# Kernel optimization log

Measured on AMD Instinct MI355X. Metric: run time of the kernel, lower is better.

Reference implementation:

```python
import jax, jax.numpy as jnp
import numpy as np

B, N, N2 = 4, 4096, 4096
CIN, DIM, KNN, UP = 128, 64, 20, 2
HPOS, HATT = 64, 256
EPS = 1e-5


def _group(feat, idx):
    # feat: (B,C,M), idx: (B,N,K) -> (B,C,N,K) gather of neighbor features
    return jax.vmap(lambda f, i: f[:, i])(feat, idx)


def _conv1d(w, b, x):
    # 1x1 Conv1d: w (O,C), x (B,C,N)
    return jnp.einsum('oc,bcn->bon', w, x) + b[:, None]


def _bn(x, g, be, m, v):
    # eval-mode BatchNorm2d on (B,C,N,K)
    inv = g / jnp.sqrt(v + EPS)
    return x * inv[:, None, None] + (be - m * inv)[:, None, None]


def setup_inputs() -> dict:
    key = jax.random.key(0)
    ks = jax.random.split(key, 32)
    r = lambda i, s: jax.random.normal(ks[i], s, jnp.float32)
    u = lambda i, s: jax.random.uniform(ks[i], s, jnp.float32, 0.5, 1.5)
    return {
        'pos1': r(0, (B, 3, N)),
        'query': r(1, (B, CIN, N)),
        'pos2': r(2, (B, 3, N2)),
        'key_feat': r(3, (B, CIN, N2)),
        'wq': r(4, (DIM, CIN)) * 0.05, 'bq': r(5, (DIM,)) * 0.05,
        'wk': r(6, (DIM, CIN)) * 0.05, 'bk': r(7, (DIM,)) * 0.05,
        'wv': r(8, (DIM, CIN)) * 0.05, 'bv': r(9, (DIM,)) * 0.05,
        'pw1': r(10, (HPOS, 3)) * 0.2, 'pb1': r(11, (HPOS,)) * 0.05,
        'pg': u(12, (HPOS,)), 'pbt': r(13, (HPOS,)) * 0.05,
        'pm': r(14, (HPOS,)) * 0.05, 'pv': u(15, (HPOS,)),
        'pw2': r(16, (DIM, HPOS)) * 0.1, 'pb2': r(17, (DIM,)) * 0.05,
        'aw1': r(18, (HATT, DIM)) * 0.1, 'ab1': r(19, (HATT,)) * 0.05,
        'ag': u(20, (HATT,)), 'abt2': r(21, (HATT,)) * 0.05,
        'am': r(22, (HATT,)) * 0.05, 'av': u(23, (HATT,)),
        'awt': r(24, (HATT, DIM, UP)) * 0.05, 'abt': r(25, (DIM,)) * 0.05,
        'we': r(26, (CIN, DIM)) * 0.1, 'be': r(27, (CIN,)) * 0.05,
    }


def reference(pos1, query, pos2, key_feat, wq, bq, wk, bk, wv, bv,
              pw1, pb1, pg, pbt, pm, pv, pw2, pb2,
              aw1, ab1, ag, abt2, am, av, awt, abt, we, be):
    q = _conv1d(wq, bq, query)          # (B,DIM,N)
    k = _conv1d(wk, bk, key_feat)       # (B,DIM,N2)
    v = _conv1d(wv, bv, key_feat)       # (B,DIM,N2)
    # KNN of pos1 queries into pos2 support set
    p1 = pos1.transpose(0, 2, 1)        # (B,N,3)
    p2 = pos2.transpose(0, 2, 1)        # (B,N2,3)
    d = (jnp.sum(p1 * p1, -1)[:, :, None] + jnp.sum(p2 * p2, -1)[:, None, :]
         - 2.0 * jnp.einsum('bnd,bmd->bnm', p1, p2))
    _, idx = jax.lax.top_k(-d, KNN)     # (B,N,KNN)
    kg = _group(k, idx)                 # (B,DIM,N,K)
    qk_rel = q[:, :, :, None] - kg
    pos_rel = pos1[:, :, :, None] - _group(pos2, idx)   # (B,3,N,K)
    # pos_mlp: conv2d 3->HPOS, BN, ReLU, conv2d HPOS->DIM
    pe = jnp.einsum('oc,bcnk->bonk', pw1, pos_rel) + pb1[:, None, None]
    pe = jax.nn.relu(_bn(pe, pg, pbt, pm, pv))
    pe = jnp.einsum('oc,bcnk->bonk', pw2, pe) + pb2[:, None, None]  # (B,DIM,N,K)
    # attn_mlp: conv2d DIM->HATT, BN, ReLU, ConvTranspose2d HATT->DIM kernel (UP,1)
    h = qk_rel + pe
    a = jnp.einsum('oc,bcnk->bonk', aw1, h) + ab1[:, None, None]
    a = jax.nn.relu(_bn(a, ag, abt2, am, av))               # (B,HATT,N,K)
    att = jnp.einsum('bcnk,cor->bonrk', a, awt).reshape(B, DIM, N * UP, KNN)
    att = att + abt[:, None, None]
    att = jax.nn.softmax(att, axis=-1)
    vg = _group(v, idx) + pe            # (B,DIM,N,K)
    vu = jnp.repeat(vg, UP, axis=2)     # nearest upsample -> (B,DIM,N*UP,K)
    agg = jnp.sum(att * vu, axis=-1)    # (B,DIM,N*UP)
    y = _conv1d(we, be, agg)            # (B,CIN,N*UP)
    identity = jnp.repeat(query, UP, axis=2)  # residual (in==out -> Identity)
    return y + identity
```

## Files before the change

### kernel.cpp

```cpp
#include <hip/hip_runtime.h>
#include <hip/hip_bf16.h>

#define BATCH 4
#define NPTS  4096
#define NPTS2 4096
#define CIN   128
#define DIM   64
#define KNN   20
#define UPF   2
#define HPOS  64
#define HATT  256
#define MOUT  8192
#define EPSF  1e-5f
#define QPB   3
#define BPB   1366

typedef _Float16 h16x8 __attribute__((ext_vector_type(8)));
typedef _Float16 h16x4 __attribute__((ext_vector_type(4)));
typedef _Float16 h16x2 __attribute__((ext_vector_type(2)));
typedef float    f32x4 __attribute__((ext_vector_type(4)));

__device__ inline float rdlane(float v, int src) {
  return __int_as_float(__builtin_amdgcn_readlane(__float_as_int(v), src));
}

__device__ __forceinline__ float distf(float qn, float m2x, float m2y, float m2z,
                                       float x, float y, float z) {
  float s = __fmaf_rn(x, x, qn);
  s = __fmaf_rn(y, y, s);
  s = __fmaf_rn(z, z, s);
  s = __fmaf_rn(m2x, x, s);
  s = __fmaf_rn(m2y, y, s);
  s = __fmaf_rn(m2z, z, s);
  return s;
}

__global__ __launch_bounds__(256) void proj_q(const float* __restrict__ x,
    const float* __restrict__ wq, const float* __restrict__ bq,
    float* __restrict__ q_t) {
  __shared__ float X[CIN][64];
  __shared__ float O[64][65];
  const int b  = blockIdx.x >> 6;
  const int n0 = (blockIdx.x & 63) * 64;
  const int t  = threadIdx.x;
  for (int l = t; l < CIN * 64; l += 256) {
    int c = l >> 6, i = l & 63;
    X[c][i] = x[(b * CIN + c) * NPTS + n0 + i];
  }
  __syncthreads();
  const int n_l = t & 63;
  const int w   = __builtin_amdgcn_readfirstlane(t >> 6);
  float acc[16];
#pragma unroll
  for (int i = 0; i < 16; ++i) acc[i] = bq[w * 16 + i];
  for (int c = 0; c < CIN; ++c) {
    float xv = X[c][n_l];
#pragma unroll
    for (int i = 0; i < 16; ++i) acc[i] += wq[(w * 16 + i) * CIN + c] * xv;
  }
#pragma unroll
  for (int i = 0; i < 16; ++i) O[n_l][w * 16 + i] = acc[i];
  __syncthreads();
  for (int l = t; l < 64 * 64; l += 256)
    q_t[(b * NPTS + n0 + (l >> 6)) * DIM + (l & 63)] = O[l >> 6][l & 63];
}

__global__ __launch_bounds__(256) void proj_kv(const float* __restrict__ x,
    const float* __restrict__ wk, const float* __restrict__ bk,
    const float* __restrict__ wv, const float* __restrict__ bv,
    float* __restrict__ k_t, float* __restrict__ v_t) {
  __shared__ float X[CIN][64];
  __shared__ float O[64][65];
  const int b  = blockIdx.x >> 6;
  const int n0 = (blockIdx.x & 63) * 64;
  const int t  = threadIdx.x;
  for (int l = t; l < CIN * 64; l += 256) {
    int c = l >> 6, i = l & 63;
    X[c][i] = x[(b * CIN + c) * NPTS2 + n0 + i];
  }
  __syncthreads();
  const int n_l = t & 63;
  const int w   = __builtin_amdgcn_readfirstlane(t >> 6);
  float acck[16], accv[16];
#pragma unroll
  for (int i = 0; i < 16; ++i) { acck[i] = bk[w * 16 + i]; accv[i] = bv[w * 16 + i]; }
  for (int c = 0; c < CIN; ++c) {
    float xv = X[c][n_l];
#pragma unroll
    for (int i = 0; i < 16; ++i) {
      acck[i] += wk[(w * 16 + i) * CIN + c] * xv;
      accv[i] += wv[(w * 16 + i) * CIN + c] * xv;
    }
  }
#pragma unroll
  for (int i = 0; i < 16; ++i) O[n_l][w * 16 + i] = acck[i];
  __syncthreads();
  for (int l = t; l < 64 * 64; l += 256)
    k_t[(b * NPTS2 + n0 + (l >> 6)) * DIM + (l & 63)] = O[l >> 6][l & 63];
  __syncthreads();
#pragma unroll
  for (int i = 0; i < 16; ++i) O[n_l][w * 16 + i] = accv[i];
  __syncthreads();
  for (int l = t; l < 64 * 64; l += 256)
    v_t[(b * NPTS2 + n0 + (l >> 6)) * DIM + (l & 63)] = O[l >> 6][l & 63];
}

__global__ __launch_bounds__(256) void knn_kernel(const float* __restrict__ pos1,
    const float* __restrict__ pos2, int* __restrict__ idxout) {
  __shared__ int   cntS[4];
  __shared__ float dbufS[4][64];
  __shared__ int   jbufS[4][64];
  const int lane = threadIdx.x & 63;
  const int wv   = threadIdx.x >> 6;
  const int g    = blockIdx.x * 4 + wv;
  const int b    = g >> 12;
  const int n    = g & (NPTS - 1);
  const float qx = pos1[(b * 3 + 0) * NPTS + n];
  const float qy = pos1[(b * 3 + 1) * NPTS + n];
  const float qz = pos1[(b * 3 + 2) * NPTS + n];
  const float qn = qx * qx + qy * qy + qz * qz;
  const float m2x = -2.0f * qx, m2y = -2.0f * qy, m2z = -2.0f * qz;
  const float* p2x = pos2 + (b * 3 + 0) * NPTS2;
  const float* p2y = pos2 + (b * 3 + 1) * NPTS2;
  const float* p2z = pos2 + (b * 3 + 2) * NPTS2;

  float mymin = 3.402823466e38f;
  for (int j0 = 0; j0 < NPTS2; j0 += 64) {
    int j = j0 + lane;
    float d = distf(qn, m2x, m2y, m2z, p2x[j], p2y[j], p2z[j]);
    mymin = fminf(mymin, d);
  }
  float v = mymin;
#pragma unroll
  for (int k = 2; k <= 64; k <<= 1) {
#pragma unroll
    for (int jj = k >> 1; jj >= 1; jj >>= 1) {
      float o = __shfl_xor(v, jj);
      bool up = ((lane & k) == 0);
      bool keepmin = (((lane & jj) == 0) == up);
      v = keepmin ? fminf(v, o) : fmaxf(v, o);
    }
  }
  const float T0 = rdlane(v, 19);

  if (lane == 0) cntS[wv] = 0;
  __syncthreads();

  for (int j0 = 0; j0 < NPTS2; j0 += 64) {
    int j = j0 + lane;
    float d = distf(qn, m2x, m2y, m2z, p2x[j], p2y[j], p2z[j]);
    if (d <= T0) {
      int slot = atomicAdd(&cntS[wv], 1);
      if (slot < 64) { dbufS[wv][slot] = d; jbufS[wv][slot] = j; }
    }
  }
  __syncthreads();

  const int cnt = cntS[wv];
  if (cnt <= 64) {
    float dk = (lane < cnt) ? dbufS[wv][lane] : 3.402823466e38f;
    int   jk = (lane < cnt) ? jbufS[wv][lane] : 0x7fffffff;
#pragma unroll
    for (int k = 2; k <= 64; k <<= 1) {
#pragma unroll
      for (int jj = k >> 1; jj >= 1; jj >>= 1) {
        float od = __shfl_xor(dk, jj);
        int   oj = __shfl_xor(jk, jj);
        bool mineSm = (dk < od) || (dk == od && jk < oj);
        bool up = ((lane & k) == 0);
        bool keepmin = (((lane & jj) == 0) == up);
        bool takeOther = (keepmin != mineSm);
        dk = takeOther ? od : dk;
        jk = takeOther ? oj : jk;
      }
    }
    if (lane < KNN) idxout[(b * NPTS + n) * KNN + lane] = jk;
  } else {
    float dl = 3.402823466e38f;
    int   il = 0;
    for (int j0 = 0; j0 < NPTS2; j0 += 64) {
      int j = j0 + lane;
      float d = distf(qn, m2x, m2y, m2z, p2x[j], p2y[j], p2z[j]);
      float T = rdlane(dl, 19);
      unsigned long long m = __ballot(d < T);
      while (m) {
        int src = __ffsll(m) - 1;
        m &= m - 1;
        float dd = rdlane(d, src);
        float T2 = rdlane(dl, 19);
        if (dd < T2) {
          int jj2 = j0 + src;
          float pd = __shfl_up(dl, 1);
          int   pi = __shfl_up(il, 1);
          if (dl > dd) {
            if (lane == 0 || pd <= dd) { dl = dd; il = jj2; }
            else                       { dl = pd; il = pi; }
          }
        }
      }
    }
    if (lane < KNN) idxout[(b * NPTS + n) * KNN + lane] = il;
  }
}

__global__ __launch_bounds__(256) void pack_weights(
    const float* __restrict__ aw1, const float* __restrict__ awt,
    const float* __restrict__ pw2,
    const float* __restrict__ ag,  const float* __restrict__ av,
    const float* __restrict__ abt2, const float* __restrict__ am,
    const float* __restrict__ abt,
    const float* __restrict__ pg,  const float* __restrict__ pv,
    const float* __restrict__ pbt, const float* __restrict__ pm,
    const float* __restrict__ ab1, const float* __restrict__ pb1,
    const float* __restrict__ pw1,
    _Float16* __restrict__ aw1h, _Float16* __restrict__ awtP,
    _Float16* __restrict__ pw2h, float* __restrict__ abtX,
    float* __restrict__ ab1f, float* __restrict__ pw1f,
    float* __restrict__ pb1f) {
  int i = blockIdx.x * 256 + threadIdx.x;
  if (i < 16384) {
    int j = i >> 6;
    float inv = ag[j] / sqrtf(av[j] + EPSF);
    aw1h[i] = (_Float16)(aw1[i] * inv);
  }
  if (i < 32768) {
    int orr = i >> 8, j = i & 255;
    awtP[i] = (_Float16)awt[j * 128 + orr];
  }
  if (i < 4096) pw2h[i] = (_Float16)pw2[i];
  if (i < 256) {
    float inv = ag[i] / sqrtf(av[i] + EPSF);
    ab1f[i] = ab1[i] * inv + (abt2[i] - am[i] * inv);
  }
  if (i < 192) {
    int hc = i / 3;
    float inv = pg[hc] / sqrtf(pv[hc] + EPSF);
    pw1f[i] = pw1[i] * inv;
  }
  if (i < 128) abtX[i] = abt[i >> 1];
  if (i < 64) {
    float inv = pg[i] / sqrtf(pv[i] + EPSF);
    pb1f[i] = pb1[i] * inv + (pbt[i] - pm[i] * inv);
  }
}

#define SM_R0    0
#define SM_R1    9216
#define SM_BUF1  18432
#define SM_LGC   0
#define SM_VGB   27648

__global__ __launch_bounds__(256, 4) void attn_mfma(
    const float* __restrict__ q_t, const float* __restrict__ k_t,
    const float* __restrict__ v_t, const int* __restrict__ idx,
    const float* __restrict__ pos1, const float* __restrict__ pos2,
    const float* __restrict__ pw1f, const float* __restrict__ pb1f,
    const _Float16* __restrict__ pw2h, const float* __restrict__ pb2,
    const _Float16* __restrict__ aw1h, const float* __restrict__ ab1f,
    const _Float16* __restrict__ awtP, const float* __restrict__ abtX,
    float* __restrict__ agg) {
  __shared__ __align__(16) char smem[36352];
  const int b  = blockIdx.x / BPB;
  const int n0 = (blockIdx.x - b * BPB) * QPB;
  const int t  = threadIdx.x;
  const int lane = t & 63;
  const int w  = t >> 6;
  const int r  = lane & 15;
  const int q4 = lane >> 4;

  const int colB = t & 63, cgB = t >> 6;
  const int pB = colB / 20, kkB = colB - pB * 20;
  const bool okB = (pB < QPB) && (n0 + pB < NPTS);
  const int nqB = okB ? (n0 + pB) : 0;
  int jB = 0;
  if (okB) jB = idx[(b * NPTS + nqB) * KNN + kkB];

  f32x4 qv4[4], kv4[4], vv4[4];
  {
    const float* qrow = q_t + ((size_t)(b * NPTS  + nqB)) * DIM + cgB * 16;
    const float* krow = k_t + ((size_t)(b * NPTS2 + jB))  * DIM + cgB * 16;
    const float* vrow = v_t + ((size_t)(b * NPTS2 + jB))  * DIM + cgB * 16;
#pragma unroll
    for (int u = 0; u < 4; ++u) {
      qv4[u] = *(const f32x4*)(qrow + u * 4);
      kv4[u] = *(const f32x4*)(krow + u * 4);
      vv4[u] = *(const f32x4*)(vrow + u * 4);
    }
  }

  {
    float p0 = 0.f, p1 = 0.f, p2 = 0.f;
    if (okB) {
      p0 = pos1[(b * 3 + 0) * NPTS + nqB] - pos2[(b * 3 + 0) * NPTS2 + jB];
      p1 = pos1[(b * 3 + 1) * NPTS + nqB] - pos2[(b * 3 + 1) * NPTS2 + jB];
      p2 = pos1[(b * 3 + 2) * NPTS + nqB] - pos2[(b * 3 + 2) * NPTS2 + jB];
    }
#pragma unroll
    for (int ii = 0; ii < 16; ii += 2) {
      int hc = cgB * 16 + ii;
      float v0 = pb1f[hc]     + pw1f[hc*3]   * p0 + pw1f[hc*3+1] * p1 + pw1f[hc*3+2] * p2;
      float v1 = pb1f[hc + 1] + pw1f[hc*3+3] * p0 + pw1f[hc*3+4] * p1 + pw1f[hc*3+5] * p2;
      v0 = fmaxf(v0, 0.f);
      v1 = fmaxf(v1, 0.f);
      if (!okB) { v0 = 0.f; v1 = 0.f; }
      h16x2 pk = {(_Float16)v0, (_Float16)v1};
      *(h16x2*)(smem + SM_R0 + ((colB * 72 + hc) * 2)) = pk;
    }
  }
  __syncthreads();

  {
    h16x8 a0[2];
#pragma unroll
    for (int ks = 0; ks < 2; ++ks)
      a0[ks] = *(const h16x8*)&pw2h[(w * 16 + r) * 64 + ks * 32 + q4 * 8];
    f32x4 acc[4];
#pragma unroll
    for (int nt = 0; nt < 4; ++nt) acc[nt] = (f32x4){0.f, 0.f, 0.f, 0.f};
#pragma unroll
    for (int ks = 0; ks < 2; ++ks)
#pragma unroll
      for (int nt = 0; nt < 4; ++nt) {
        h16x8 bv = *(h16x8*)(smem + SM_R0 + ((nt * 16 + r) * 72 + ks * 32 + q4 * 8) * 2);
        acc[nt] = __builtin_amdgcn_mfma_f32_16x16x32_f16(a0[ks], bv, acc[nt], 0, 0, 0);
      }
    int o0 = w * 16 + q4 * 4;
    f32x4 pbv = *(const f32x4*)&pb2[o0];
#pragma unroll
    for (int nt = 0; nt < 4; ++nt) {
      f32x4 vv = acc[nt] + pbv;
      h16x4 pk = {(_Float16)vv[0], (_Float16)vv[1], (_Float16)vv[2], (_Float16)vv[3]};
      *(h16x4*)(smem + SM_R1 + ((nt * 16 + r) * 72 + o0) * 2) = pk;
    }
  }

  {
#pragma unroll
    for (int u = 0; u < 4; ++u) {
      int c0 = cgB * 16 + u * 4;
      h16x4 peh = *(h16x4*)(smem + SM_R1 + (colB * 72 + c0) * 2);
      f32x4 pe = {(float)peh[0], (float)peh[1], (float)peh[2], (float)peh[3]};
      f32x4 hv = qv4[u] - kv4[u] + pe;
      f32x4 gv = vv4[u] + pe;
      if (!okB) { hv = (f32x4){0.f,0.f,0.f,0.f}; gv = hv; }
      h16x4 hp = {(_Float16)hv[0], (_Float16)hv[1], (_Float16)hv[2], (_Float16)hv[3]};
      h16x4 gp = {(_Float16)gv[0], (_Float16)gv[1], (_Float16)gv[2], (_Float16)gv[3]};
      *(h16x4*)(smem + SM_R1  + (colB * 72 + c0) * 2) = hp;
      *(h16x4*)(smem + SM_VGB + (colB * 68 + c0) * 2) = gp;
    }
  }
  __syncthreads();

  h16x8 bs[2][4];
#pragma unroll
  for (int ks = 0; ks < 2; ++ks)
#pragma unroll
    for (int nt = 0; nt < 4; ++nt)
      bs[ks][nt] = *(h16x8*)(smem + SM_R1 + ((nt * 16 + r) * 72 + ks * 32 + q4 * 8) * 2);

  f32x4 accD[2][4];
#pragma unroll
  for (int h = 0; h < 2; ++h)
#pragma unroll
    for (int nt = 0; nt < 4; ++nt) accD[h][nt] = (f32x4){0.f, 0.f, 0.f, 0.f};

#define C_QUARTER(quar, base)                                                  \
  {                                                                            \
    int mt = (quar) * 4 + w;                                                   \
    h16x8 af0 = *(const h16x8*)&aw1h[(mt * 16 + r) * 64 + q4 * 8];             \
    h16x8 af1 = *(const h16x8*)&aw1h[(mt * 16 + r) * 64 + 32 + q4 * 8];        \
    f32x4 acc[4];                                                              \
    _Pragma("unroll")                                                          \
    for (int nt = 0; nt < 4; ++nt) acc[nt] = (f32x4){0.f, 0.f, 0.f, 0.f};      \
    _Pragma("unroll")                                                          \
    for (int nt = 0; nt < 4; ++nt)                                             \
      acc[nt] = __builtin_amdgcn_mfma_f32_16x16x32_f16(af0, bs[0][nt], acc[nt], 0, 0, 0); \
    _Pragma("unroll")                                                          \
    for (int nt = 0; nt < 4; ++nt)                                             \
      acc[nt] = __builtin_amdgcn_mfma_f32_16x16x32_f16(af1, bs[1][nt], acc[nt], 0, 0, 0); \
    int j0  = mt * 16 + q4 * 4;                                                \
    int jq0 = j0 - (quar) * 64;                                                \
    f32x4 b1 = *(const f32x4*)&ab1f[j0];                                       \
    _Pragma("unroll")                                                          \
    for (int nt = 0; nt < 4; ++nt) {                                           \
      int col = nt * 16 + r;                                                   \
      float v0 = fmaxf(acc[nt][0] + b1[0], 0.f);                               \
      float v1 = fmaxf(acc[nt][1] + b1[1], 0.f);                               \
      float v2 = fmaxf(acc[nt][2] + b1[2], 0.f);                               \
      float v3 = fmaxf(acc[nt][3] + b1[3], 0.f);                               \
      h16x4 pk = {(_Float16)v0, (_Float16)v1, (_Float16)v2, (_Float16)v3};     \
      *(h16x4*)(smem + (base) + (col * 72 + jq0) * 2) = pk;                    \
    }                                                                          \
  }

#define D_QUARTER(quar, base)                                                  \
  {                                                                            \
    _Pragma("unroll")                                                          \
    for (int ks2 = 0; ks2 < 2; ++ks2) {                                        \
      h16x8 bsv[4];                                                            \
      _Pragma("unroll")                                                        \
      for (int nt = 0; nt < 4; ++nt)                                           \
        bsv[nt] = *(h16x8*)(smem + (base) + ((nt * 16 + r) * 72 + ks2 * 32 + q4 * 8) * 2); \
      int ksg = (quar) * 2 + ks2;                                              \
      _Pragma("unroll")                                                        \
      for (int h = 0; h < 2; ++h) {                                            \
        int mt2 = w * 2 + h;                                                   \
        h16x8 af = *(const h16x8*)&awtP[(mt2 * 16 + r) * 256 + ksg * 32 + q4 * 8]; \
        _Pragma("unroll")                                                      \
        for (int nt = 0; nt < 4; ++nt)                                         \
          accD[h][nt] = __builtin_amdgcn_mfma_f32_16x16x32_f16(af, bsv[nt], accD[h][nt], 0, 0, 0); \
      }                                                                        \
    }                                                                          \
  }

  C_QUARTER(0, SM_R0)
  __syncthreads();
  D_QUARTER(0, SM_R0)
  C_QUARTER(1, SM_BUF1)
  __syncthreads();
  D_QUARTER(1, SM_BUF1)
  C_QUARTER(2, SM_R0)
  __syncthreads();
  D_QUARTER(2, SM_R0)
  C_QUARTER(3, SM_BUF1)
  __syncthreads();
  D_QUARTER(3, SM_BUF1)

  {
#pragma unroll
    for (int h = 0; h < 2; ++h) {
      int orr0 = (w * 2 + h) * 16 + q4 * 4;
      f32x4 ab = *(const f32x4*)&abtX[orr0];
#pragma unroll
      for (int nt = 0; nt < 4; ++nt) {
        int col = nt * 16 + r;
        if (col < QPB * KNN) {
          f32x4 vv = accD[h][nt] + ab;
          h16x4 pk = {(_Float16)vv[0], (_Float16)vv[1], (_Float16)vv[2], (_Float16)vv[3]};
          *(h16x4*)(smem + SM_LGC + (col * 136 + orr0) * 2) = pk;
        }
      }
    }
  }
  __syncthreads();

  if (t < 64 * QPB) {
    int li = t & 63, p = t >> 6;
    if (n0 + p < NPTS) {
#pragma unroll
      for (int half = 0; half < 2; ++half) {
        int orr = (li >> 4) * 32 + half * 16 + (li & 15);
        int o = orr >> 1, rb = orr & 1;
        float L[KNN];
#pragma unroll
        for (int kk = 0; kk < KNN; ++kk)
          L[kk] = (float)*(_Float16*)(smem + SM_LGC + (((p * 20 + kk) * 136 + orr) * 2));
        float mx = L[0];
#pragma unroll
        for (int kk = 1; kk < KNN; ++kk) mx = fmaxf(mx, L[kk]);
        float s = 0.f;
#pragma unroll
        for (int kk = 0; kk < KNN; ++kk) { L[kk] = __expf(L[kk] - mx); s += L[kk]; }
        float rs = 1.0f / s;
        float a = 0.f;
#pragma unroll
        for (int kk = 0; kk < KNN; ++kk) {
          _Float16 gv = *(_Float16*)(smem + SM_VGB + (((p * 20 + kk) * 68 + o) * 2));
          a += L[kk] * (float)gv;
        }
        agg[(((size_t)(b * NPTS + n0 + p)) * UPF + rb) * DIM + o] = a * rs;
      }
    }
  }
#undef C_QUARTER
#undef D_QUARTER
}

__global__ __launch_bounds__(256) void out_proj(const float* __restrict__ agg,
    const float* __restrict__ we, const float* __restrict__ be,
    const float* __restrict__ query, float* __restrict__ out) {
  __shared__ float A[64][65];
  const int b  = blockIdx.x >> 7;
  const int m0 = (blockIdx.x & 127) * 64;
  const int t  = threadIdx.x;
  for (int l = t; l < 64 * 64; l += 256) {
    int row = l >> 6, c = l & 63;
    A[row][c] = agg[(b * MOUT + m0 + row) * DIM + c];
  }
  __syncthreads();
  const int m_l = t & 63;
  const int w   = __builtin_amdgcn_readfirstlane(t >> 6);
  float acc[32];
#pragma unroll
  for (int i = 0; i < 32; ++i) acc[i] = 0.f;
  for (int c = 0; c < DIM; ++c) {
    float a = A[m_l][c];
#pragma unroll
    for (int i = 0; i < 32; ++i) acc[i] += we[(w * 32 + i) * DIM + c] * a;
  }
  const int m = m0 + m_l;
#pragma unroll
  for (int i = 0; i < 32; ++i) {
    int o = w * 32 + i;
    out[(b * CIN + o) * MOUT + m] = acc[i] + be[o] + query[(b * CIN + o) * NPTS + (m >> 1)];
  }
}

extern "C" void kernel_launch(void* const* d_in, const int* in_sizes, int n_in,
                              void* d_out, int out_size, void* d_ws, size_t ws_size,
                              hipStream_t stream) {
  (void)in_sizes; (void)n_in; (void)out_size; (void)ws_size;
  const float* pos1     = (const float*)d_in[0];
  const float* query    = (const float*)d_in[1];
  const float* pos2     = (const float*)d_in[2];
  const float* key_feat = (const float*)d_in[3];
  const float* wq  = (const float*)d_in[4];
  const float* bq  = (const float*)d_in[5];
  const float* wk  = (const float*)d_in[6];
  const float* bk  = (const float*)d_in[7];
  const float* wv  = (const float*)d_in[8];
  const float* bv  = (const float*)d_in[9];
  const float* pw1 = (const float*)d_in[10];
  const float* pb1 = (const float*)d_in[11];
  const float* pg  = (const float*)d_in[12];
  const float* pbt = (const float*)d_in[13];
  const float* pm  = (const float*)d_in[14];
  const float* pv  = (const float*)d_in[15];
  const float* pw2 = (const float*)d_in[16];
  const float* pb2 = (const float*)d_in[17];
  const float* aw1 = (const float*)d_in[18];
  const float* ab1 = (const float*)d_in[19];
  const float* ag  = (const float*)d_in[20];
  const float* abt2= (const float*)d_in[21];
  const float* am  = (const float*)d_in[22];
  const float* av  = (const float*)d_in[23];
  const float* awt = (const float*)d_in[24];
  const float* abt = (const float*)d_in[25];
  const float* we  = (const float*)d_in[26];
  const float* be  = (const float*)d_in[27];

  float* ws   = (float*)d_ws;
  float* q_t  = ws;
  float* k_t  = q_t + BATCH * NPTS * DIM;
  float* v_t  = k_t + BATCH * NPTS2 * DIM;
  float* aggb = v_t + BATCH * NPTS2 * DIM;
  int*   idxb = (int*)(aggb + BATCH * MOUT * DIM);
  _Float16* aw1h = (_Float16*)(idxb + BATCH * NPTS * KNN);
  _Float16* awtP = aw1h + HATT * DIM;
  _Float16* pw2h = awtP + 128 * HATT;
  float* abtX    = (float*)(pw2h + DIM * HPOS);
  float* ab1f    = abtX + 128;
  float* pw1f    = ab1f + HATT;
  float* pb1f    = pw1f + HPOS * 3;

  pack_weights<<<128, 256, 0, stream>>>(aw1, awt, pw2, ag, av, abt2, am, abt,
      pg, pv, pbt, pm, ab1, pb1, pw1,
      aw1h, awtP, pw2h, abtX, ab1f, pw1f, pb1f);
  proj_q <<<BATCH * (NPTS / 64), 256, 0, stream>>>(query, wq, bq, q_t);
  proj_kv<<<BATCH * (NPTS2 / 64), 256, 0, stream>>>(key_feat, wk, bk, wv, bv, k_t, v_t);
  knn_kernel<<<BATCH * NPTS / 4, 256, 0, stream>>>(pos1, pos2, idxb);
  attn_mfma<<<BATCH * BPB, 256, 0, stream>>>(q_t, k_t, v_t, idxb, pos1, pos2,
      pw1f, pb1f, pw2h, pb2, aw1h, ab1f, awtP, abtX, aggb);
  out_proj<<<BATCH * (MOUT / 64), 256, 0, stream>>>(aggb, we, be, query, (float*)d_out);
}
```

Before: 381.2 us.

## Shrink attention kernel LDS footprint and raise occupancy, vectorize LDS stores and softmax

Drops the separate second staging buffer by reusing the R1 region for the odd quarters, moving the value buffer down and cutting shared memory from about 36KB to 27KB, with launch bounds raised to 6 blocks per SM. Adds an extra barrier before the logits overwrite so the reused region stays safe. Replaces narrow h16x2/h16x4 LDS writes with 16-byte h16x8 stores. The softmax is restructured so each thread reads its paired logits and value column once and fuses the exp/sum/weighted-accumulate loop. This also changes which output channel each thread owns, and the higher occupancy target may force register spills.

```diff
diff --git a/kernel.cpp b/kernel.cpp
--- a/kernel.cpp
+++ b/kernel.cpp
@@ -246,11 +246,10 @@
 
 #define SM_R0    0
 #define SM_R1    9216
-#define SM_BUF1  18432
 #define SM_LGC   0
-#define SM_VGB   27648
-
-__global__ __launch_bounds__(256, 4) void attn_mfma(
+#define SM_VGB   18432
+
+__global__ __launch_bounds__(256, 6) void attn_mfma(
     const float* __restrict__ q_t, const float* __restrict__ k_t,
     const float* __restrict__ v_t, const int* __restrict__ idx,
     const float* __restrict__ pos1, const float* __restrict__ pos2,
@@ -259,7 +258,7 @@
     const _Float16* __restrict__ aw1h, const float* __restrict__ ab1f,
     const _Float16* __restrict__ awtP, const float* __restrict__ abtX,
     float* __restrict__ agg) {
-  __shared__ __align__(16) char smem[36352];
+  __shared__ __align__(16) char smem[27136];
   const int b  = blockIdx.x / BPB;
   const int n0 = (blockIdx.x - b * BPB) * QPB;
   const int t  = threadIdx.x;
@@ -296,15 +295,17 @@
       p2 = pos1[(b * 3 + 2) * NPTS + nqB] - pos2[(b * 3 + 2) * NPTS2 + jB];
     }
 #pragma unroll
-    for (int ii = 0; ii < 16; ii += 2) {
-      int hc = cgB * 16 + ii;
-      float v0 = pb1f[hc]     + pw1f[hc*3]   * p0 + pw1f[hc*3+1] * p1 + pw1f[hc*3+2] * p2;
-      float v1 = pb1f[hc + 1] + pw1f[hc*3+3] * p0 + pw1f[hc*3+4] * p1 + pw1f[hc*3+5] * p2;
-      v0 = fmaxf(v0, 0.f);
-      v1 = fmaxf(v1, 0.f);
-      if (!okB) { v0 = 0.f; v1 = 0.f; }
-      h16x2 pk = {(_Float16)v0, (_Float16)v1};
-      *(h16x2*)(smem + SM_R0 + ((colB * 72 + hc) * 2)) = pk;
+    for (int hf = 0; hf < 2; ++hf) {
+      h16x8 pk;
+#pragma unroll
+      for (int ii = 0; ii < 8; ++ii) {
+        int hc = cgB * 16 + hf * 8 + ii;
+        float v0 = pb1f[hc] + pw1f[hc*3] * p0 + pw1f[hc*3+1] * p1 + pw1f[hc*3+2] * p2;
+        v0 = fmaxf(v0, 0.f);
+        if (!okB) v0 = 0.f;
+        pk[ii] = (_Float16)v0;
+      }
+      *(h16x8*)(smem + SM_R0 + ((colB * 72 + cgB * 16 + hf * 8) * 2)) = pk;
     }
   }
   __syncthreads();
@@ -335,19 +336,29 @@
   }
 
   {
+    h16x8 pe8[2];
+#pragma unroll
+    for (int hf = 0; hf < 2; ++hf)
+      pe8[hf] = *(h16x8*)(smem + SM_R1 + (colB * 72 + cgB * 16 + hf * 8) * 2);
+    h16x8 hp8[2];
 #pragma unroll
     for (int u = 0; u < 4; ++u) {
-      int c0 = cgB * 16 + u * 4;
-      h16x4 peh = *(h16x4*)(smem + SM_R1 + (colB * 72 + c0) * 2);
-      f32x4 pe = {(float)peh[0], (float)peh[1], (float)peh[2], (float)peh[3]};
+      int hf = u >> 1, e0 = (u & 1) * 4;
+      f32x4 pe = {(float)pe8[hf][e0],     (float)pe8[hf][e0 + 1],
+                  (float)pe8[hf][e0 + 2], (float)pe8[hf][e0 + 3]};
       f32x4 hv = qv4[u] - kv4[u] + pe;
       f32x4 gv = vv4[u] + pe;
       if (!okB) { hv = (f32x4){0.f,0.f,0.f,0.f}; gv = hv; }
-      h16x4 hp = {(_Float16)hv[0], (_Float16)hv[1], (_Float16)hv[2], (_Float16)hv[3]};
+      hp8[hf][e0]     = (_Float16)hv[0];
+      hp8[hf][e0 + 1] = (_Float16)hv[1];
+      hp8[hf][e0 + 2] = (_Float16)hv[2];
+      hp8[hf][e0 + 3] = (_Float16)hv[3];
       h16x4 gp = {(_Float16)gv[0], (_Float16)gv[1], (_Float16)gv[2], (_Float16)gv[3]};
-      *(h16x4*)(smem + SM_R1  + (colB * 72 + c0) * 2) = hp;
-      *(h16x4*)(smem + SM_VGB + (colB * 68 + c0) * 2) = gp;
-    }
+      *(h16x4*)(smem + SM_VGB + (colB * 68 + cgB * 16 + u * 4) * 2) = gp;
+    }
+#pragma unroll
+    for (int hf = 0; hf < 2; ++hf)
+      *(h16x8*)(smem + SM_R1 + (colB * 72 + cgB * 16 + hf * 8) * 2) = hp8[hf];
   }
   __syncthreads();
 
@@ -416,15 +427,16 @@
   C_QUARTER(0, SM_R0)
   __syncthreads();
   D_QUARTER(0, SM_R0)
-  C_QUARTER(1, SM_BUF1)
-  __syncthreads();
-  D_QUARTER(1, SM_BUF1)
+  C_QUARTER(1, SM_R1)
+  __syncthreads();
+  D_QUARTER(1, SM_R1)
   C_QUARTER(2, SM_R0)
   __syncthreads();
   D_QUARTER(2, SM_R0)
-  C_QUARTER(3, SM_BUF1)
-  __syncthreads();
-  D_QUARTER(3, SM_BUF1)
+  C_QUARTER(3, SM_R1)
+  __syncthreads();
+  D_QUARTER(3, SM_R1)
+  __syncthreads();
 
   {
 #pragma unroll
@@ -447,28 +459,27 @@
   if (t < 64 * QPB) {
     int li = t & 63, p = t >> 6;
     if (n0 + p < NPTS) {
+      h16x2 Lp[KNN];
+      float G[KNN];
+#pragma unroll
+      for (int kk = 0; kk < KNN; ++kk) {
+        Lp[kk] = *(h16x2*)(smem + SM_LGC + ((p * 20 + kk) * 136 + li * 2) * 2);
+        G[kk]  = (float)*(_Float16*)(smem + SM_VGB + ((p * 20 + kk) * 68 + li) * 2);
+      }
 #pragma unroll
       for (int half = 0; half < 2; ++half) {
-        int orr = (li >> 4) * 32 + half * 16 + (li & 15);
-        int o = orr >> 1, rb = orr & 1;
-        float L[KNN];
-#pragma unroll
-        for (int kk = 0; kk < KNN; ++kk)
-          L[kk] = (float)*(_Float16*)(smem + SM_LGC + (((p * 20 + kk) * 136 + orr) * 2));
-        float mx = L[0];
-#pragma unroll
-        for (int kk = 1; kk < KNN; ++kk) mx = fmaxf(mx, L[kk]);
-        float s = 0.f;
-#pragma unroll
-        for (int kk = 0; kk < KNN; ++kk) { L[kk] = __expf(L[kk] - mx); s += L[kk]; }
+        float mx = (float)Lp[0][half];
+#pragma unroll
+        for (int kk = 1; kk < KNN; ++kk) mx = fmaxf(mx, (float)Lp[kk][half]);
+        float s = 0.f, a = 0.f;
+#pragma unroll
+        for (int kk = 0; kk < KNN; ++kk) {
+          float e = __expf((float)Lp[kk][half] - mx);
+          s += e;
+          a += e * G[kk];
+        }
         float rs = 1.0f / s;
-        float a = 0.f;
-#pragma unroll
-        for (int kk = 0; kk < KNN; ++kk) {
-          _Float16 gv = *(_Float16*)(smem + SM_VGB + (((p * 20 + kk) * 68 + o) * 2));
-          a += L[kk] * (float)gv;
-        }
-        agg[(((size_t)(b * NPTS + n0 + p)) * UPF + rb) * DIM + o] = a * rs;
+        agg[(((size_t)(b * NPTS + n0 + p)) * UPF + half) * DIM + li] = a * rs;
       }
     }
   }
```

Result: slower. 498.3 us (+30.7%).
